# Kernel optimization log

Hardware: AMD Instinct MI355X
Metric: run time of the kernel (lower is better)

The kernel has to match this reference:

```python
import jax, jax.numpy as jnp
import numpy as np

EMBED = 1024
HEADS = 16
HEAD_DIM = EMBED // HEADS


def setup_inputs() -> dict:
    key = jax.random.key(0)
    ks = jax.random.split(key, 5)
    s = 0.02
    x = jax.random.normal(ks[0], (2, 2048, EMBED), dtype=jnp.float32)
    W_qkv = jax.random.normal(ks[1], (EMBED, 3 * EMBED), dtype=jnp.float32) * s
    b_qkv = jnp.zeros((3 * EMBED,), dtype=jnp.float32)
    W_proj = jax.random.normal(ks[2], (EMBED, EMBED), dtype=jnp.float32) * s
    b_proj = jnp.zeros((EMBED,), dtype=jnp.float32)
    return {"x": x, "W_qkv": W_qkv, "b_qkv": b_qkv, "W_proj": W_proj, "b_proj": b_proj}


def reference(x, W_qkv, b_qkv, W_proj, b_proj):
    B, N, _ = x.shape
    scale = HEAD_DIM ** -0.5
    qkv = x @ W_qkv + b_qkv                     # [B,N,3E]
    qkv = qkv.reshape(B, N, 3, HEADS, HEAD_DIM)
    q = qkv[:, :, 0].transpose(0, 2, 1, 3) * scale  # [B,H,N,D]
    k = qkv[:, :, 1].transpose(0, 2, 1, 3)
    v = qkv[:, :, 2].transpose(0, 2, 1, 3)
    attn = jnp.einsum('bhnd,bhmd->bhnm', q, k)  # [B,H,N,N]
    attn = jax.nn.softmax(attn, axis=-1)
    out = jnp.einsum('bhnm,bhmd->bhnd', attn, v)  # [B,H,N,D]
    out = out.transpose(0, 2, 1, 3).reshape(B, N, HEADS * HEAD_DIM)
    return out @ W_proj + b_proj
```

## Files before the change

### kernel.cpp

```cpp
#include <hip/hip_runtime.h>
#include <hip/hip_bf16.h>
#include <stdint.h>

typedef unsigned short u16;
typedef __bf16 bf16x8 __attribute__((ext_vector_type(8)));
typedef float f32x4 __attribute__((ext_vector_type(4)));

__device__ __forceinline__ u16 f2bf(float f) {
    union { float f; unsigned u; } x; x.f = f;
    unsigned u = x.u;
    u += 0x7FFFu + ((u >> 16) & 1u);
    return (u16)(u >> 16);
}
__device__ __forceinline__ float bf2f(u16 h) {
    union { unsigned u; float f; } x; x.u = ((unsigned)h) << 16; return x.f;
}

typedef __attribute__((address_space(1))) void gvoid;
typedef __attribute__((address_space(3))) void lvoid;
__device__ __forceinline__ void gl2lds16(const void* g, void* l) {
    __builtin_amdgcn_global_load_lds((gvoid*)g, (lvoid*)l, 16, 0, 0);
}

__global__ __launch_bounds__(256) void prep_kernel(
    const float* __restrict__ x, u16* __restrict__ xb,
    const float* __restrict__ Wqkv, u16* __restrict__ wqkvT,
    const float* __restrict__ Wproj, u16* __restrict__ wprojT)
{
    __shared__ u16 tile[64][65];
    const int blk = blockIdx.x;
    const int tid = threadIdx.x;

    if (blk < 2048) {
        const size_t i = ((size_t)blk * 256 + tid) * 8;
        float4 a = *(const float4*)(x + i);
        float4 b = *(const float4*)(x + i + 4);
        ushort4 oa, ob;
        oa.x = f2bf(a.x); oa.y = f2bf(a.y); oa.z = f2bf(a.z); oa.w = f2bf(a.w);
        ob.x = f2bf(b.x); ob.y = f2bf(b.y); ob.z = f2bf(b.z); ob.w = f2bf(b.w);
        *(ushort4*)(xb + i) = oa;
        *(ushort4*)(xb + i + 4) = ob;
        return;
    }
    const float* in; u16* out; int rows, cols, bx, by;
    if (blk < 2816) { int t = blk - 2048; in = Wqkv;  out = wqkvT;  rows = 1024; cols = 3072; bx = t % 48; by = t / 48; }
    else            { int t = blk - 2816; in = Wproj; out = wprojT; rows = 1024; cols = 1024; bx = t % 16; by = t / 16; }
#pragma unroll
    for (int i = 0; i < 16; i++) {
        int e = i * 256 + tid;
        int r = e >> 6, c = e & 63;
        tile[r][c] = f2bf(in[(size_t)(by * 64 + r) * cols + bx * 64 + c]);
    }
    __syncthreads();
#pragma unroll
    for (int i = 0; i < 16; i++) {
        int e = i * 256 + tid;
        int r = e >> 6, c = e & 63;
        out[(size_t)(bx * 64 + r) * rows + by * 64 + c] = tile[c][r];
    }
}

__global__ __launch_bounds__(256) void gemm_qkv(
    const u16* __restrict__ A, const u16* __restrict__ Bt,
    const float* __restrict__ bias,
    u16* __restrict__ q, u16* __restrict__ ko, u16* __restrict__ vt)
{
    constexpr int K = 1024;
    __shared__ __align__(16) u16 smem[128 * 132];
    u16* sA = smem;
    u16* sB = smem + 8192;
    const int tid = threadIdx.x;
    const int wave = tid >> 6, lane = tid & 63;
    const int quad = lane >> 4, l16 = lane & 15;
    const int wm = (wave >> 1) * 64, wn = (wave & 1) * 64;
    const int m0 = blockIdx.y * 128, n0 = blockIdx.x * 128;
    const int srow = lane >> 3;
    const int scol = (lane & 7) * 8;

    f32x4 acc[4][4];
#pragma unroll
    for (int i = 0; i < 4; i++)
#pragma unroll
        for (int j = 0; j < 4; j++)
#pragma unroll
            for (int r = 0; r < 4; r++) acc[i][j][r] = 0.f;

    for (int kt = 0; kt < K; kt += 64) {
        __syncthreads();
#pragma unroll
        for (int t = 0; t < 4; t++) {
            int rb = wave * 32 + t * 8;
            gl2lds16(A  + (size_t)(m0 + rb + srow) * K + kt + scol, &sA[rb * 64]);
            gl2lds16(Bt + (size_t)(n0 + rb + srow) * K + kt + scol, &sB[rb * 64]);
        }
        __syncthreads();
#pragma unroll
        for (int kk = 0; kk < 64; kk += 32) {
            bf16x8 af[4], bfr[4];
#pragma unroll
            for (int t = 0; t < 4; t++) {
                af[t]  = *(const bf16x8*)&sA[(wm + t * 16 + l16) * 64 + kk + quad * 8];
                bfr[t] = *(const bf16x8*)&sB[(wn + t * 16 + l16) * 64 + kk + quad * 8];
            }
#pragma unroll
            for (int i = 0; i < 4; i++)
#pragma unroll
                for (int j = 0; j < 4; j++)
                    acc[i][j] = __builtin_amdgcn_mfma_f32_16x16x32_bf16(
                        af[i], bfr[j], acc[i][j], 0, 0, 0);
        }
    }

    const float QSCALE = 0.18033688011112042f;
    const float sc = (n0 < 1024) ? QSCALE : 1.0f;
    __syncthreads();
#pragma unroll
    for (int i = 0; i < 4; i++) {
#pragma unroll
        for (int j = 0; j < 4; j++) {
            float bv = bias[n0 + wn + j * 16 + l16];
#pragma unroll
            for (int r = 0; r < 4; r++) {
                float v = (acc[i][j][r] + bv) * sc;
                smem[(wm + i * 16 + quad * 4 + r) * 132 + wn + j * 16 + l16] = f2bf(v);
            }
        }
    }
    __syncthreads();

    if (n0 < 2048) {
        u16* dst = (n0 < 1024) ? q : ko;
#pragma unroll
        for (int it = 0; it < 8; it++) {
            int c = it * 256 + tid;
            int m_l = c >> 4;
            int n8 = (c & 15) * 8;
            uint4 w = *(const uint4*)&smem[m_l * 132 + n8];
            int n = n0 + n8;
            int h = (n & 1023) >> 6, d = n & 63;
            int m = m0 + m_l;
            int b = m >> 11, t = m & 2047;
            *(uint4*)(dst + ((size_t)(b * 16 + h) * 2048 + t) * 64 + d) = w;
        }
    } else {
        int nv = n0 - 2048;
        int n_l = tid & 127, mh = tid >> 7;
        int hh = (nv >> 6) + (n_l >> 6);
        int d = n_l & 63;
        int bb = m0 >> 11, t0 = m0 & 2047;
        u16* vrow = vt + ((size_t)(bb * 16 + hh) * 64 + d) * 2048 + t0 + mh * 64;
#pragma unroll
        for (int it = 0; it < 8; it++) {
            int tch = mh * 64 + it * 8;
            union { u16 s[8]; uint4 w; } pk;
#pragma unroll
            for (int i = 0; i < 8; i++)
                pk.s[i] = smem[(tch + i) * 132 + n_l];
            *(uint4*)(vrow + it * 8) = pk.w;
        }
    }
}

__global__ __launch_bounds__(256) void attn_kernel(
    const u16* __restrict__ q, const u16* __restrict__ ko,
    const u16* __restrict__ vt,
    u16* __restrict__ op0, u16* __restrict__ op1,
    float* __restrict__ lp0, float* __restrict__ lp1)
{
    __shared__ __align__(16) u16 sQP[128 * 72];
    __shared__ __align__(16) u16 sK[64 * 72];
    __shared__ __align__(16) u16 sV[64 * 72];

    const int tid = threadIdx.x;
    const int wave = tid >> 6, lane = tid & 63;
    const int quad = lane >> 4, l16 = lane & 15;

    const int lid = blockIdx.x;
    const int xcd = lid & 7, idx = lid >> 3;
    const int h = xcd * 2 + (idx & 1);
    const int b = (idx >> 1) & 1;
    const int q0 = ((idx >> 2) & 15) * 128;
    const int khalf = idx >> 6;
    const int kbase = khalf * 1024;
    const size_t bh = (size_t)(b * 16 + h);

    const u16* qp  = q  + bh * 2048 * 64;
    const u16* kp  = ko + bh * 2048 * 64;
    const u16* vtp = vt + bh * 64 * 2048;

    const int sr0 = tid >> 3;
    const int sc0 = (tid & 7) * 8;
    const int sr1 = sr0 + 32;

#pragma unroll
    for (int i = 0; i < 4; i++) {
        int c = tid + i * 256;
        int r = c >> 3, cc = c & 7;
        *(uint4*)&sQP[r * 72 + cc * 8] =
            *(const uint4*)(qp + (size_t)(q0 + r) * 64 + cc * 8);
    }

    union { uint32_t u[4]; bf16x8 v; } ones;
    ones.u[0] = ones.u[1] = ones.u[2] = ones.u[3] = 0x3F803F80u;

    uint4 pk0 = *(const uint4*)(kp + (size_t)(kbase + sr0) * 64 + sc0);
    uint4 pk1 = *(const uint4*)(kp + (size_t)(kbase + sr1) * 64 + sc0);
    uint4 pv0 = *(const uint4*)(vtp + (size_t)sr0 * 2048 + kbase + sc0);
    uint4 pv1 = *(const uint4*)(vtp + (size_t)sr1 * 2048 + kbase + sc0);

    __syncthreads();

    bf16x8 qf[2][2];
#pragma unroll
    for (int i = 0; i < 2; i++)
#pragma unroll
        for (int k2 = 0; k2 < 2; k2++)
            qf[i][k2] = *(const bf16x8*)&sQP[(wave * 32 + i * 16 + l16) * 72 + k2 * 32 + quad * 8];
    __syncthreads();

    f32x4 accO[2][4];
    f32x4 accL[2];
#pragma unroll
    for (int i = 0; i < 2; i++) {
#pragma unroll
        for (int r = 0; r < 4; r++) accL[i][r] = 0.f;
#pragma unroll
        for (int j = 0; j < 4; j++)
#pragma unroll
            for (int r = 0; r < 4; r++) accO[i][j][r] = 0.f;
    }

    for (int kt = kbase; kt < kbase + 1024; kt += 64) {
        __syncthreads();
        *(uint4*)&sK[sr0 * 72 + sc0] = pk0;
        *(uint4*)&sK[sr1 * 72 + sc0] = pk1;
        *(uint4*)&sV[sr0 * 72 + sc0] = pv0;
        *(uint4*)&sV[sr1 * 72 + sc0] = pv1;
        if (kt + 64 < kbase + 1024) {
            int nt = kt + 64;
            pk0 = *(const uint4*)(kp + (size_t)(nt + sr0) * 64 + sc0);
            pk1 = *(const uint4*)(kp + (size_t)(nt + sr1) * 64 + sc0);
            pv0 = *(const uint4*)(vtp + (size_t)sr0 * 2048 + nt + sc0);
            pv1 = *(const uint4*)(vtp + (size_t)sr1 * 2048 + nt + sc0);
        }
        __syncthreads();

        f32x4 S[2][4];
#pragma unroll
        for (int i = 0; i < 2; i++)
#pragma unroll
            for (int j = 0; j < 4; j++)
#pragma unroll
                for (int r = 0; r < 4; r++) S[i][j][r] = 0.f;
#pragma unroll
        for (int k2 = 0; k2 < 2; k2++) {
            int kk = k2 * 32;
#pragma unroll
            for (int j = 0; j < 4; j++) {
                bf16x8 bk = *(const bf16x8*)&sK[(j * 16 + l16) * 72 + kk + quad * 8];
                S[0][j] = __builtin_amdgcn_mfma_f32_16x16x32_bf16(qf[0][k2], bk, S[0][j], 0, 0, 0);
                S[1][j] = __builtin_amdgcn_mfma_f32_16x16x32_bf16(qf[1][k2], bk, S[1][j], 0, 0, 0);
            }
        }

        u16* pw = &sQP[(wave * 32 + quad * 4) * 72 + l16];
#pragma unroll
        for (int i = 0; i < 2; i++)
#pragma unroll
            for (int j = 0; j < 4; j++)
#pragma unroll
                for (int r = 0; r < 4; r++) {
                    union { float f; uint32_t u; } e;
                    e.f = __builtin_amdgcn_exp2f(S[i][j][r]);
                    pw[(i * 16 + r) * 72 + j * 16] = (u16)(e.u >> 16);
                }

#pragma unroll
        for (int k2 = 0; k2 < 2; k2++) {
            int kk = k2 * 32;
            bf16x8 bv[4];
#pragma unroll
            for (int j = 0; j < 4; j++)
                bv[j] = *(const bf16x8*)&sV[(j * 16 + l16) * 72 + kk + quad * 8];
#pragma unroll
            for (int i = 0; i < 2; i++) {
                bf16x8 ap = *(const bf16x8*)&sQP[(wave * 32 + i * 16 + l16) * 72 + kk + quad * 8];
#pragma unroll
                for (int j = 0; j < 4; j++)
                    accO[i][j] = __builtin_amdgcn_mfma_f32_16x16x32_bf16(ap, bv[j], accO[i][j], 0, 0, 0);
                accL[i] = __builtin_amdgcn_mfma_f32_16x16x32_bf16(ap, ones.v, accL[i], 0, 0, 0);
            }
        }
    }

    u16* op = khalf ? op1 : op0;
    float* lp = khalf ? lp1 : lp0;
#pragma unroll
    for (int i = 0; i < 2; i++)
#pragma unroll
        for (int r = 0; r < 4; r++) {
            int t = q0 + wave * 32 + i * 16 + quad * 4 + r;
            if (l16 == 0) lp[bh * 2048 + t] = accL[i][r];
            size_t row = (size_t)b * 2048 + t;
#pragma unroll
            for (int j = 0; j < 4; j++)
                op[row * 1024 + h * 64 + j * 16 + l16] = f2bf(accO[i][j][r]);
        }
}

__global__ __launch_bounds__(256) void combine_kernel(
    const u16* __restrict__ op0, const u16* __restrict__ op1,
    const float* __restrict__ lp0, const float* __restrict__ lp1,
    u16* __restrict__ ob)
{
    const size_t i = ((size_t)blockIdx.x * 256 + threadIdx.x) * 8;
    int m = (int)(i >> 10), e = (int)(i & 1023);
    int b = m >> 11, t = m & 2047, h = e >> 6;
    float inv = 1.f / (lp0[(size_t)(b * 16 + h) * 2048 + t] +
                       lp1[(size_t)(b * 16 + h) * 2048 + t]);
    union { uint4 w; u16 s[8]; } a, c, o;
    a.w = *(const uint4*)(op0 + i);
    c.w = *(const uint4*)(op1 + i);
#pragma unroll
    for (int k = 0; k < 8; k++)
        o.s[k] = f2bf((bf2f(a.s[k]) + bf2f(c.s[k])) * inv);
    *(uint4*)(ob + i) = o.w;
}

__global__ __launch_bounds__(256) void gemm_proj(
    const u16* __restrict__ A, const u16* __restrict__ Bt,
    const float* __restrict__ bias, float* __restrict__ out)
{
    constexpr int K = 1024;
    __shared__ __align__(16) u16 sA[64 * 64];
    __shared__ __align__(16) u16 sB[128 * 64];
    const int tid = threadIdx.x;
    const int wave = tid >> 6, lane = tid & 63;
    const int quad = lane >> 4, l16 = lane & 15;
    const int wm = (wave & 1) * 32, wn = (wave >> 1) * 64;

    const int lid = blockIdx.x;
    const int xcd = lid & 7, idx = lid >> 3;
    const int m0 = (xcd * 8 + (idx & 7)) * 64;
    const int n0 = (idx >> 3) * 128;

    const int srow = lane >> 3;
    const int scol = (lane & 7) * 8;

    f32x4 acc[2][4];
#pragma unroll
    for (int i = 0; i < 2; i++)
#pragma unroll
        for (int j = 0; j < 4; j++)
#pragma unroll
            for (int r = 0; r < 4; r++) acc[i][j][r] = 0.f;

    for (int kt = 0; kt < K; kt += 64) {
        __syncthreads();
#pragma unroll
        for (int t = 0; t < 2; t++) {
            int rb = wave * 16 + t * 8;
            gl2lds16(A + (size_t)(m0 + rb + srow) * K + kt + scol, &sA[rb * 64]);
        }
#pragma unroll
        for (int t = 0; t < 4; t++) {
            int rb = wave * 32 + t * 8;
            gl2lds16(Bt + (size_t)(n0 + rb + srow) * K + kt + scol, &sB[rb * 64]);
        }
        __syncthreads();
#pragma unroll
        for (int kk = 0; kk < 64; kk += 32) {
            bf16x8 af[2], bfr[4];
#pragma unroll
            for (int t = 0; t < 2; t++)
                af[t] = *(const bf16x8*)&sA[(wm + t * 16 + l16) * 64 + kk + quad * 8];
#pragma unroll
            for (int t = 0; t < 4; t++)
                bfr[t] = *(const bf16x8*)&sB[(wn + t * 16 + l16) * 64 + kk + quad * 8];
#pragma unroll
            for (int i = 0; i < 2; i++)
#pragma unroll
                for (int j = 0; j < 4; j++)
                    acc[i][j] = __builtin_amdgcn_mfma_f32_16x16x32_bf16(
                        af[i], bfr[j], acc[i][j], 0, 0, 0);
        }
    }

#pragma unroll
    for (int i = 0; i < 2; i++) {
#pragma unroll
        for (int j = 0; j < 4; j++) {
            int n = n0 + wn + j * 16 + l16;
            float bv = bias[n];
#pragma unroll
            for (int r = 0; r < 4; r++) {
                int m = m0 + wm + i * 16 + quad * 4 + r;
                out[(size_t)m * 1024 + n] = acc[i][j][r] + bv;
            }
        }
    }
}

extern "C" void kernel_launch(void* const* d_in, const int* in_sizes, int n_in,
                              void* d_out, int out_size, void* d_ws, size_t ws_size,
                              hipStream_t stream) {
    const float* x     = (const float*)d_in[0];
    const float* Wqkv  = (const float*)d_in[1];
    const float* bqkv  = (const float*)d_in[2];
    const float* Wproj = (const float*)d_in[3];
    const float* bproj = (const float*)d_in[4];
    float* out = (float*)d_out;
    char* ws = (char*)d_ws;

    u16* wqkvT  = (u16*)(ws);
    u16* wprojT = (u16*)(ws +  6291456);
    u16* xb     = (u16*)(ws +  8388608);
    u16* qb     = (u16*)(ws + 16777216);
    u16* kb     = (u16*)(ws + 25165824);
    u16* vtb    = (u16*)(ws + 33554432);
    u16* ob     = (u16*)(ws + 41943040);

    u16*   op0 = ob;
    u16*   op1 = xb;
    float* lp0 = (float*)wqkvT;
    float* lp1 = (float*)(ws + 262144);

    prep_kernel<<<dim3(3072), 256, 0, stream>>>(x, xb, Wqkv, wqkvT, Wproj, wprojT);
    gemm_qkv<<<dim3(24, 32), 256, 0, stream>>>(xb, wqkvT, bqkv, qb, kb, vtb);
    attn_kernel<<<dim3(1024), 256, 0, stream>>>(qb, kb, vtb, op0, op1, lp0, lp1);
    combine_kernel<<<dim3(2048), 256, 0, stream>>>(op0, op1, lp0, lp1, ob);
    gemm_proj<<<dim3(512), 256, 0, stream>>>(ob, wprojT, bproj, out);
}
```

Baseline: 212.6 us.

## Rewrite attention inner loop with 32x32 MFMA and register-resident P

Switches the QK^T and PV matmuls from 16x16x32 to 32x32x16 MFMA, computing S transposed (K as the A operand) so each lane can pack exp(S) straight into the PV A operand without an LDS round trip. The row sum is now accumulated in registers with one cross-half shuffle, replacing the extra MFMA against a ones vector. Q is loaded directly from global memory into registers, and K/V go into double-buffered LDS. It also adds an occupancy hint of 4 blocks per CU. P is now rounded to nearest instead of truncated, and the new register layout may raise register pressure.

```diff
diff --git a/kernel.cpp b/kernel.cpp
--- a/kernel.cpp
+++ b/kernel.cpp
@@ -5,6 +5,7 @@
 typedef unsigned short u16;
 typedef __bf16 bf16x8 __attribute__((ext_vector_type(8)));
 typedef float f32x4 __attribute__((ext_vector_type(4)));
+typedef float f32x16 __attribute__((ext_vector_type(16)));
 
 __device__ __forceinline__ u16 f2bf(float f) {
     union { float f; unsigned u; } x; x.f = f;
@@ -161,19 +162,18 @@
     }
 }
 
-__global__ __launch_bounds__(256) void attn_kernel(
+__global__ __launch_bounds__(256, 4) void attn_kernel(
     const u16* __restrict__ q, const u16* __restrict__ ko,
     const u16* __restrict__ vt,
     u16* __restrict__ op0, u16* __restrict__ op1,
     float* __restrict__ lp0, float* __restrict__ lp1)
 {
-    __shared__ __align__(16) u16 sQP[128 * 72];
-    __shared__ __align__(16) u16 sK[64 * 72];
-    __shared__ __align__(16) u16 sV[64 * 72];
+    __shared__ __align__(16) u16 sK[2][64 * 72];
+    __shared__ __align__(16) u16 sV[2][64 * 72];
 
     const int tid = threadIdx.x;
     const int wave = tid >> 6, lane = tid & 63;
-    const int quad = lane >> 4, l16 = lane & 15;
+    const int l31 = lane & 31, hi = lane >> 5;
 
     const int lid = blockIdx.x;
     const int xcd = lid & 7, idx = lid >> 3;
@@ -188,56 +188,40 @@
     const u16* kp  = ko + bh * 2048 * 64;
     const u16* vtp = vt + bh * 64 * 2048;
 
+    bf16x8 qf[4];
+    {
+        const u16* qrow = qp + (size_t)(q0 + wave * 32 + l31) * 64 + hi * 8;
+#pragma unroll
+        for (int d = 0; d < 4; d++)
+            qf[d] = *(const bf16x8*)(qrow + d * 16);
+    }
+
     const int sr0 = tid >> 3;
     const int sc0 = (tid & 7) * 8;
     const int sr1 = sr0 + 32;
-
-#pragma unroll
-    for (int i = 0; i < 4; i++) {
-        int c = tid + i * 256;
-        int r = c >> 3, cc = c & 7;
-        *(uint4*)&sQP[r * 72 + cc * 8] =
-            *(const uint4*)(qp + (size_t)(q0 + r) * 64 + cc * 8);
-    }
-
-    union { uint32_t u[4]; bf16x8 v; } ones;
-    ones.u[0] = ones.u[1] = ones.u[2] = ones.u[3] = 0x3F803F80u;
 
     uint4 pk0 = *(const uint4*)(kp + (size_t)(kbase + sr0) * 64 + sc0);
     uint4 pk1 = *(const uint4*)(kp + (size_t)(kbase + sr1) * 64 + sc0);
     uint4 pv0 = *(const uint4*)(vtp + (size_t)sr0 * 2048 + kbase + sc0);
     uint4 pv1 = *(const uint4*)(vtp + (size_t)sr1 * 2048 + kbase + sc0);
 
-    __syncthreads();
-
-    bf16x8 qf[2][2];
-#pragma unroll
-    for (int i = 0; i < 2; i++)
-#pragma unroll
-        for (int k2 = 0; k2 < 2; k2++)
-            qf[i][k2] = *(const bf16x8*)&sQP[(wave * 32 + i * 16 + l16) * 72 + k2 * 32 + quad * 8];
-    __syncthreads();
-
-    f32x4 accO[2][4];
-    f32x4 accL[2];
-#pragma unroll
-    for (int i = 0; i < 2; i++) {
-#pragma unroll
-        for (int r = 0; r < 4; r++) accL[i][r] = 0.f;
-#pragma unroll
-        for (int j = 0; j < 4; j++)
-#pragma unroll
-            for (int r = 0; r < 4; r++) accO[i][j][r] = 0.f;
-    }
-
-    for (int kt = kbase; kt < kbase + 1024; kt += 64) {
-        __syncthreads();
-        *(uint4*)&sK[sr0 * 72 + sc0] = pk0;
-        *(uint4*)&sK[sr1 * 72 + sc0] = pk1;
-        *(uint4*)&sV[sr0 * 72 + sc0] = pv0;
-        *(uint4*)&sV[sr1 * 72 + sc0] = pv1;
-        if (kt + 64 < kbase + 1024) {
-            int nt = kt + 64;
+    f32x16 accO[2];
+#pragma unroll
+    for (int d = 0; d < 2; d++)
+#pragma unroll
+        for (int r = 0; r < 16; r++) accO[d][r] = 0.f;
+    float lsum = 0.f;
+
+    for (int t = 0; t < 16; ++t) {
+        const int cur = t & 1;
+        u16* sKc = &sK[cur][0];
+        u16* sVc = &sV[cur][0];
+        *(uint4*)&sKc[sr0 * 72 + sc0] = pk0;
+        *(uint4*)&sKc[sr1 * 72 + sc0] = pk1;
+        *(uint4*)&sVc[sr0 * 72 + sc0] = pv0;
+        *(uint4*)&sVc[sr1 * 72 + sc0] = pv1;
+        if (t < 15) {
+            int nt = kbase + (t + 1) * 64;
             pk0 = *(const uint4*)(kp + (size_t)(nt + sr0) * 64 + sc0);
             pk1 = *(const uint4*)(kp + (size_t)(nt + sr1) * 64 + sc0);
             pv0 = *(const uint4*)(vtp + (size_t)sr0 * 2048 + nt + sc0);
@@ -245,66 +229,60 @@
         }
         __syncthreads();
 
-        f32x4 S[2][4];
-#pragma unroll
-        for (int i = 0; i < 2; i++)
-#pragma unroll
-            for (int j = 0; j < 4; j++)
-#pragma unroll
-                for (int r = 0; r < 4; r++) S[i][j][r] = 0.f;
-#pragma unroll
-        for (int k2 = 0; k2 < 2; k2++) {
-            int kk = k2 * 32;
-#pragma unroll
-            for (int j = 0; j < 4; j++) {
-                bf16x8 bk = *(const bf16x8*)&sK[(j * 16 + l16) * 72 + kk + quad * 8];
-                S[0][j] = __builtin_amdgcn_mfma_f32_16x16x32_bf16(qf[0][k2], bk, S[0][j], 0, 0, 0);
-                S[1][j] = __builtin_amdgcn_mfma_f32_16x16x32_bf16(qf[1][k2], bk, S[1][j], 0, 0, 0);
-            }
-        }
-
-        u16* pw = &sQP[(wave * 32 + quad * 4) * 72 + l16];
-#pragma unroll
-        for (int i = 0; i < 2; i++)
-#pragma unroll
-            for (int j = 0; j < 4; j++)
-#pragma unroll
-                for (int r = 0; r < 4; r++) {
-                    union { float f; uint32_t u; } e;
-                    e.f = __builtin_amdgcn_exp2f(S[i][j][r]);
-                    pw[(i * 16 + r) * 72 + j * 16] = (u16)(e.u >> 16);
+#pragma unroll
+        for (int rb = 0; rb < 2; rb++) {
+            f32x16 S;
+#pragma unroll
+            for (int r = 0; r < 16; r++) S[r] = 0.f;
+            const u16* krd = &sKc[(rb * 32 + l31) * 72 + hi * 8];
+#pragma unroll
+            for (int d = 0; d < 4; d++) {
+                bf16x8 kf = *(const bf16x8*)(krd + d * 16);
+                S = __builtin_amdgcn_mfma_f32_32x32x16_bf16(kf, qf[d], S, 0, 0, 0);
+            }
+            float e[16];
+#pragma unroll
+            for (int r = 0; r < 16; r++) {
+                e[r] = __builtin_amdgcn_exp2f(S[r]);
+                lsum += e[r];
+            }
+#pragma unroll
+            for (int ks2 = 0; ks2 < 2; ks2++) {
+                union { unsigned u[4]; bf16x8 v; } pa;
+#pragma unroll
+                for (int s = 0; s < 4; s++) {
+                    unsigned lo = f2bf(e[ks2 * 8 + 2 * s]);
+                    unsigned hh = f2bf(e[ks2 * 8 + 2 * s + 1]);
+                    pa.u[s] = lo | (hh << 16);
                 }
-
-#pragma unroll
-        for (int k2 = 0; k2 < 2; k2++) {
-            int kk = k2 * 32;
-            bf16x8 bv[4];
-#pragma unroll
-            for (int j = 0; j < 4; j++)
-                bv[j] = *(const bf16x8*)&sV[(j * 16 + l16) * 72 + kk + quad * 8];
-#pragma unroll
-            for (int i = 0; i < 2; i++) {
-                bf16x8 ap = *(const bf16x8*)&sQP[(wave * 32 + i * 16 + l16) * 72 + kk + quad * 8];
-#pragma unroll
-                for (int j = 0; j < 4; j++)
-                    accO[i][j] = __builtin_amdgcn_mfma_f32_16x16x32_bf16(ap, bv[j], accO[i][j], 0, 0, 0);
-                accL[i] = __builtin_amdgcn_mfma_f32_16x16x32_bf16(ap, ones.v, accL[i], 0, 0, 0);
-            }
-        }
+                const int nb = rb * 32 + ks2 * 16 + 4 * hi;
+#pragma unroll
+                for (int db = 0; db < 2; db++) {
+                    const u16* vr = &sVc[(db * 32 + l31) * 72 + nb];
+                    union { uint2 w[2]; bf16x8 v; } vf;
+                    vf.w[0] = *(const uint2*)(vr);
+                    vf.w[1] = *(const uint2*)(vr + 8);
+                    accO[db] = __builtin_amdgcn_mfma_f32_32x32x16_bf16(pa.v, vf.v, accO[db], 0, 0, 0);
+                }
+            }
+        }
+        __syncthreads();
     }
 
     u16* op = khalf ? op1 : op0;
     float* lp = khalf ? lp1 : lp0;
-#pragma unroll
-    for (int i = 0; i < 2; i++)
-#pragma unroll
-        for (int r = 0; r < 4; r++) {
-            int t = q0 + wave * 32 + i * 16 + quad * 4 + r;
-            if (l16 == 0) lp[bh * 2048 + t] = accL[i][r];
-            size_t row = (size_t)b * 2048 + t;
-#pragma unroll
-            for (int j = 0; j < 4; j++)
-                op[row * 1024 + h * 64 + j * 16 + l16] = f2bf(accO[i][j][r]);
+
+    float ltot = lsum + __shfl_xor(lsum, 32, 64);
+    int qq0 = q0 + wave * 32;
+    if (hi == 0) lp[bh * 2048 + qq0 + l31] = ltot;
+
+#pragma unroll
+    for (int db = 0; db < 2; db++)
+#pragma unroll
+        for (int r = 0; r < 16; r++) {
+            int tq = qq0 + (r & 3) + 8 * (r >> 2) + 4 * hi;
+            size_t row = (size_t)b * 2048 + tq;
+            op[row * 1024 + h * 64 + db * 32 + l31] = f2bf(accO[db][r]);
         }
 }
 
```

Result: faster. 206.0 us (-3.1%).
